# Kernel tuning notes

Hardware: AMD Instinct MI355X
Metric: run time of the kernel (lower is better)

## Reference

```python
import jax, jax.numpy as jnp
import numpy as np

N_NODES = 50000
N_EDGES = 800000
D_IN, D_HID, D_OUT = 64, 128, 64


def _glorot(key, fan_in, fan_out):
    lim = (6.0 / (fan_in + fan_out)) ** 0.5
    return jax.random.uniform(key, (fan_in, fan_out), jnp.float32, -lim, lim)


def setup_inputs() -> dict:
    key = jax.random.key(0)
    ks = jax.random.split(key, 10)
    x = jax.random.normal(ks[0], (N_NODES, D_IN), jnp.float32)
    edge_index = jax.random.randint(ks[1], (2, N_EDGES), 0, N_NODES, jnp.int64)
    # GINConv1 MLP: Linear(D_IN->D_HID), ReLU, Linear(D_HID->D_HID)
    W1a = _glorot(ks[2], D_IN, D_HID); b1a = jnp.zeros((D_HID,), jnp.float32)
    W1b = _glorot(ks[3], D_HID, D_HID); b1b = jnp.zeros((D_HID,), jnp.float32)
    # GINConv2 MLP: Linear(D_HID->D_HID), ReLU, Linear(D_HID->D_OUT)
    W2a = _glorot(ks[4], D_HID, D_HID); b2a = jnp.zeros((D_HID,), jnp.float32)
    W2b = _glorot(ks[5], D_HID, D_OUT); b2b = jnp.zeros((D_OUT,), jnp.float32)
    return {"x": x, "edge_index": edge_index,
            "W1a": W1a, "b1a": b1a, "W1b": W1b, "b1b": b1b,
            "W2a": W2a, "b2a": b2a, "W2b": W2b, "b2b": b2b}


def _gin_conv(x, src, dst, Wa, ba, Wb, bb):
    # GIN aggregation (eps = 0): h_i = x_i + sum_{j in N(i)} x_j
    msgs = x[src]                                   # [E, d] gather
    agg = jax.ops.segment_sum(msgs, dst, num_segments=x.shape[0])  # [N, d]
    h = x + agg
    # 2-layer MLP
    h = jax.nn.relu(h @ Wa + ba)
    return h @ Wb + bb


def reference(x, edge_index, W1a, b1a, W1b, b1b, W2a, b2a, W2b, b2b):
    src, dst = edge_index[0], edge_index[1]
    h = jax.nn.relu(_gin_conv(x, src, dst, W1a, b1a, W1b, b1b))
    h = jax.nn.relu(_gin_conv(h, src, dst, W2a, b2a, W2b, b2b))
    return h
```

## Files before the change

kernel.cpp:

```cpp
#include <hip/hip_runtime.h>

#define N_NODES 50000
#define N_EDGES 800000

typedef __attribute__((ext_vector_type(8))) short short8;
typedef __attribute__((ext_vector_type(4))) float floatx4;

static __device__ __forceinline__ unsigned short f2b(float f) {
    unsigned int u = __float_as_uint(f);
    unsigned int r = u + 0x7fffu + ((u >> 16) & 1u);
    return (unsigned short)(r >> 16);
}
static __device__ __forceinline__ unsigned int pk(float a, float b) {
    return (unsigned)f2b(a) | ((unsigned)f2b(b) << 16);
}
static __device__ __forceinline__ float blo(unsigned int u) {
    return __uint_as_float(u << 16);
}
static __device__ __forceinline__ float bhi(unsigned int u) {
    return __uint_as_float(u & 0xffff0000u);
}

__global__ void hist_kernel(const int* __restrict__ dst, int* __restrict__ deg,
                            int n) {
    int i = blockIdx.x * blockDim.x + threadIdx.x;
    if (i < n) atomicAdd(&deg[dst[i]], 1);
}

__global__ __launch_bounds__(1024) void scanA_kernel(
    const int* __restrict__ deg, int* __restrict__ bsum, int n) {
    __shared__ int s[1024];
    const int tid = threadIdx.x;
    int i = blockIdx.x * 1024 + tid;
    s[tid] = (i < n) ? deg[i] : 0;
    __syncthreads();
    for (int d = 512; d > 0; d >>= 1) {
        if (tid < d) s[tid] += s[tid + d];
        __syncthreads();
    }
    if (tid == 0) bsum[blockIdx.x] = s[0];
}

__global__ __launch_bounds__(64) void scanB_kernel(int* __restrict__ bsum,
                                                   int nb) {
    const int tid = threadIdx.x;
    int v = (tid < nb) ? bsum[tid] : 0;
    for (int d = 1; d < 64; d <<= 1) {
        int t = __shfl_up(v, d, 64);
        if (tid >= d) v += t;
    }
    int excl = __shfl_up(v, 1, 64);
    if (tid == 0) excl = 0;
    if (tid < nb) bsum[tid] = excl;
}

__global__ __launch_bounds__(1024) void scanC_kernel(
    const int* __restrict__ deg, const int* __restrict__ bpref,
    int* __restrict__ off, int* __restrict__ cursor, int n) {
    __shared__ int s[1024];
    const int tid = threadIdx.x;
    const int i = blockIdx.x * 1024 + tid;
    const int v = (i < n) ? deg[i] : 0;
    s[tid] = v;
    __syncthreads();
    for (int d = 1; d < 1024; d <<= 1) {
        int t = (tid >= d) ? s[tid - d] : 0;
        __syncthreads();
        s[tid] += t;
        __syncthreads();
    }
    const int excl = s[tid] - v + bpref[blockIdx.x];
    if (i < n) {
        off[i] = excl;
        cursor[i] = excl;
        if (i == n - 1) off[n] = excl + v;
    }
}

__global__ void fill_kernel(const int* __restrict__ src,
                            const int* __restrict__ dst,
                            int* __restrict__ cursor,
                            unsigned short* __restrict__ nbr, int n) {
    int i = blockIdx.x * blockDim.x + threadIdx.x;
    if (i < n) {
        int pos = atomicAdd(&cursor[dst[i]], 1);
        nbr[pos] = (unsigned short)src[i];
    }
}

__global__ __launch_bounds__(256) void prep_weights_kernel(
    const float* __restrict__ W1a, const float* __restrict__ W1b,
    const float* __restrict__ W2a, const float* __restrict__ W2b,
    unsigned short* __restrict__ W1aT, unsigned short* __restrict__ W1bT,
    unsigned short* __restrict__ W2aT, unsigned short* __restrict__ W2bT) {
    int i = blockIdx.x * 256 + threadIdx.x;
    if (i < 8192) {
        int n = i >> 6, k = i & 63;
        W1aT[i] = f2b(W1a[k * 128 + n]);
    } else if (i < 24576) {
        int j = i - 8192, n = j >> 7, k = j & 127;
        W1bT[j] = f2b(W1b[k * 128 + n]);
    } else if (i < 40960) {
        int j = i - 24576, n = j >> 7, k = j & 127;
        W2aT[j] = f2b(W2a[k * 128 + n]);
    } else if (i < 49152) {
        int j = i - 40960, n = j >> 7, k = j & 127;
        W2bT[j] = f2b(W2b[k * 64 + n]);
    }
}

__global__ __launch_bounds__(256) void convert_x_kernel(
    const float* __restrict__ x, unsigned short* __restrict__ xb, int n4) {
    int i = blockIdx.x * 256 + threadIdx.x;
    if (i < n4) {
        float4 v = ((const float4*)x)[i];
        uint2 o;
        o.x = pk(v.x, v.y);
        o.y = pk(v.z, v.w);
        ((uint2*)xb)[i] = o;
    }
}

__global__ __launch_bounds__(256) void gather1_kernel(
    const unsigned short* __restrict__ xb, const int* __restrict__ off,
    const unsigned short* __restrict__ nbr, unsigned short* __restrict__ t1,
    int n_nodes) {
    const int tid = threadIdx.x;
    const int node = blockIdx.x * 16 + (tid >> 4);
    const int c = tid & 15;
    if (node >= n_nodes) return;
    const uint2* xr = (const uint2*)xb;
    const uint2 a = xr[(size_t)node * 16 + c];
    float f0 = blo(a.x), f1 = bhi(a.x), f2 = blo(a.y), f3 = bhi(a.y);
    const int lo = off[node], hi = off[node + 1];
    int j = lo;
    for (; j + 4 <= hi; j += 4) {
        const int s0 = nbr[j], s1 = nbr[j + 1], s2 = nbr[j + 2],
                  s3 = nbr[j + 3];
        const uint2 v0 = xr[(size_t)s0 * 16 + c];
        const uint2 v1 = xr[(size_t)s1 * 16 + c];
        const uint2 v2 = xr[(size_t)s2 * 16 + c];
        const uint2 v3 = xr[(size_t)s3 * 16 + c];
        f0 += (blo(v0.x) + blo(v1.x)) + (blo(v2.x) + blo(v3.x));
        f1 += (bhi(v0.x) + bhi(v1.x)) + (bhi(v2.x) + bhi(v3.x));
        f2 += (blo(v0.y) + blo(v1.y)) + (blo(v2.y) + blo(v3.y));
        f3 += (bhi(v0.y) + bhi(v1.y)) + (bhi(v2.y) + bhi(v3.y));
    }
    for (; j < hi; ++j) {
        const uint2 v = xr[(size_t)nbr[j] * 16 + c];
        f0 += blo(v.x); f1 += bhi(v.x);
        f2 += blo(v.y); f3 += bhi(v.y);
    }
    uint2 o;
    o.x = pk(f0, f1);
    o.y = pk(f2, f3);
    ((uint2*)t1)[(size_t)node * 16 + c] = o;
}

__global__ __launch_bounds__(256) void gather2_kernel(
    const unsigned short* __restrict__ h, const int* __restrict__ off,
    const unsigned short* __restrict__ nbr, unsigned short* __restrict__ t2,
    int n_nodes) {
    const int tid = threadIdx.x;
    const int node = blockIdx.x * 16 + (tid >> 4);
    const int c = tid & 15;
    if (node >= n_nodes) return;
    const uint4* hr = (const uint4*)h;
    const uint4 a = hr[(size_t)node * 16 + c];
    float f0 = blo(a.x), f1 = bhi(a.x), f2 = blo(a.y), f3 = bhi(a.y);
    float f4 = blo(a.z), f5 = bhi(a.z), f6 = blo(a.w), f7 = bhi(a.w);
    const int lo = off[node], hi = off[node + 1];
    int j = lo;
    for (; j + 4 <= hi; j += 4) {
        const int s0 = nbr[j], s1 = nbr[j + 1], s2 = nbr[j + 2],
                  s3 = nbr[j + 3];
        const uint4 v0 = hr[(size_t)s0 * 16 + c];
        const uint4 v1 = hr[(size_t)s1 * 16 + c];
        const uint4 v2 = hr[(size_t)s2 * 16 + c];
        const uint4 v3 = hr[(size_t)s3 * 16 + c];
        f0 += (blo(v0.x) + blo(v1.x)) + (blo(v2.x) + blo(v3.x));
        f1 += (bhi(v0.x) + bhi(v1.x)) + (bhi(v2.x) + bhi(v3.x));
        f2 += (blo(v0.y) + blo(v1.y)) + (blo(v2.y) + blo(v3.y));
        f3 += (bhi(v0.y) + bhi(v1.y)) + (bhi(v2.y) + bhi(v3.y));
        f4 += (blo(v0.z) + blo(v1.z)) + (blo(v2.z) + blo(v3.z));
        f5 += (bhi(v0.z) + bhi(v1.z)) + (bhi(v2.z) + bhi(v3.z));
        f6 += (blo(v0.w) + blo(v1.w)) + (blo(v2.w) + blo(v3.w));
        f7 += (bhi(v0.w) + bhi(v1.w)) + (bhi(v2.w) + bhi(v3.w));
    }
    for (; j < hi; ++j) {
        const uint4 v = hr[(size_t)nbr[j] * 16 + c];
        f0 += blo(v.x); f1 += bhi(v.x); f2 += blo(v.y); f3 += bhi(v.y);
        f4 += blo(v.z); f5 += bhi(v.z); f6 += blo(v.w); f7 += bhi(v.w);
    }
    uint4 o;
    o.x = pk(f0, f1); o.y = pk(f2, f3);
    o.z = pk(f4, f5); o.w = pk(f6, f7);
    ((uint4*)t2)[(size_t)node * 16 + c] = o;
}

template <int DIN, int DH, int DOUT, bool OUT_BF16>
__global__ __launch_bounds__(256) void mlp_mfma_kernel(
    const unsigned short* __restrict__ t, const unsigned short* __restrict__ WaT,
    const float* __restrict__ ba, const unsigned short* __restrict__ WbT,
    const float* __restrict__ bb, void* __restrict__ outp, int n_rows) {
    constexpr int SA = DIN + 16;
    constexpr int SH = DH + 16;
    __shared__ unsigned short tA[64 * SA];
    __shared__ unsigned short hidA[64 * SH];

    const int tid = threadIdx.x;
    const int row0 = blockIdx.x * 64;

    constexpr int CHUNKS = 64 * DIN / 8;
    const uint4* tg = (const uint4*)t;
    for (int i = tid; i < CHUNKS; i += 256) {
        const int row = i / (DIN / 8);
        const int cb = i % (DIN / 8);
        uint4 v = {0u, 0u, 0u, 0u};
        const int gr = row0 + row;
        if (gr < n_rows) v = tg[(size_t)gr * (DIN / 8) + cb];
        *(uint4*)&tA[row * SA + cb * 8] = v;
    }
    __syncthreads();

    const int lane = tid & 63;
    const int wv = tid >> 6;
    const int quad = lane >> 4;
    const int l16 = lane & 15;
    const int m0 = wv * 16;

    short8 a1[DIN / 32];
#pragma unroll
    for (int kk = 0; kk < DIN / 32; ++kk)
        a1[kk] = *(const short8*)&tA[(m0 + l16) * SA + kk * 32 + quad * 8];
#pragma unroll
    for (int nt = 0; nt < DH / 16; ++nt) {
        floatx4 acc = {0.f, 0.f, 0.f, 0.f};
#pragma unroll
        for (int kk = 0; kk < DIN / 32; ++kk) {
            short8 b =
                *(const short8*)&WaT[(nt * 16 + l16) * DIN + kk * 32 + quad * 8];
            acc = __builtin_amdgcn_mfma_f32_16x16x32_bf16(a1[kk], b, acc, 0, 0, 0);
        }
        const float bias = ba[nt * 16 + l16];
#pragma unroll
        for (int r = 0; r < 4; ++r) {
            const float v = fmaxf(acc[r] + bias, 0.f);
            hidA[(m0 + quad * 4 + r) * SH + nt * 16 + l16] = f2b(v);
        }
    }

    short8 a2[DH / 32];
#pragma unroll
    for (int kk = 0; kk < DH / 32; ++kk)
        a2[kk] = *(const short8*)&hidA[(m0 + l16) * SH + kk * 32 + quad * 8];
#pragma unroll
    for (int nt = 0; nt < DOUT / 16; ++nt) {
        floatx4 acc = {0.f, 0.f, 0.f, 0.f};
#pragma unroll
        for (int kk = 0; kk < DH / 32; ++kk) {
            short8 b =
                *(const short8*)&WbT[(nt * 16 + l16) * DH + kk * 32 + quad * 8];
            acc = __builtin_amdgcn_mfma_f32_16x16x32_bf16(a2[kk], b, acc, 0, 0, 0);
        }
        const float bias = bb[nt * 16 + l16];
#pragma unroll
        for (int r = 0; r < 4; ++r) {
            const float v = fmaxf(acc[r] + bias, 0.f);
            const int grow = row0 + m0 + quad * 4 + r;
            if (grow < n_rows) {
                if (OUT_BF16)
                    ((unsigned short*)outp)[(size_t)grow * DOUT + nt * 16 + l16] =
                        f2b(v);
                else
                    ((float*)outp)[(size_t)grow * DOUT + nt * 16 + l16] = v;
            }
        }
    }
}

extern "C" void kernel_launch(void* const* d_in, const int* in_sizes, int n_in,
                              void* d_out, int out_size, void* d_ws,
                              size_t ws_size, hipStream_t stream) {
    const float* x   = (const float*)d_in[0];
    const int*   ei  = (const int*)d_in[1];
    const float* W1a = (const float*)d_in[2];
    const float* b1a = (const float*)d_in[3];
    const float* W1b = (const float*)d_in[4];
    const float* b1b = (const float*)d_in[5];
    const float* W2a = (const float*)d_in[6];
    const float* b2a = (const float*)d_in[7];
    const float* W2b = (const float*)d_in[8];
    const float* b2b = (const float*)d_in[9];
    float* out = (float*)d_out;

    const int* src = ei;
    const int* dst = ei + N_EDGES;

    unsigned short* xb = (unsigned short*)d_ws;
    unsigned short* t1 = xb + (size_t)N_NODES * 64;
    unsigned short* h  = t1 + (size_t)N_NODES * 64;
    unsigned short* t2 = h + (size_t)N_NODES * 128;
    unsigned short* W1aT = t2 + (size_t)N_NODES * 128;
    unsigned short* W1bT = W1aT + 8192;
    unsigned short* W2aT = W1bT + 16384;
    unsigned short* W2bT = W2aT + 16384;
    int* deg    = (int*)(W2bT + 8192);
    int* off    = deg + N_NODES;
    int* cursor = off + N_NODES + 1;
    int* bsum   = cursor + N_NODES;
    unsigned short* nbr = (unsigned short*)(bsum + 64);

    constexpr int NB = (N_NODES + 1023) / 1024;

    hipMemsetAsync(deg, 0, N_NODES * sizeof(int), stream);
    hist_kernel<<<(N_EDGES + 255) / 256, 256, 0, stream>>>(dst, deg, N_EDGES);
    scanA_kernel<<<NB, 1024, 0, stream>>>(deg, bsum, N_NODES);
    scanB_kernel<<<1, 64, 0, stream>>>(bsum, NB);
    scanC_kernel<<<NB, 1024, 0, stream>>>(deg, bsum, off, cursor, N_NODES);
    fill_kernel<<<(N_EDGES + 255) / 256, 256, 0, stream>>>(src, dst, cursor,
                                                           nbr, N_EDGES);
    prep_weights_kernel<<<192, 256, 0, stream>>>(W1a, W1b, W2a, W2b, W1aT,
                                                 W1bT, W2aT, W2bT);
    convert_x_kernel<<<(N_NODES * 16 + 255) / 256, 256, 0, stream>>>(
        x, xb, N_NODES * 16);

    gather1_kernel<<<(N_NODES + 15) / 16, 256, 0, stream>>>(xb, off, nbr, t1,
                                                            N_NODES);
    mlp_mfma_kernel<64, 128, 128, true>
        <<<(N_NODES + 63) / 64, 256, 0, stream>>>(t1, W1aT, b1a, W1bT, b1b, h,
                                                  N_NODES);

    gather2_kernel<<<(N_NODES + 15) / 16, 256, 0, stream>>>(h, off, nbr, t2,
                                                            N_NODES);
    mlp_mfma_kernel<128, 128, 64, false>
        <<<(N_NODES + 63) / 64, 256, 0, stream>>>(t2, W2aT, b2a, W2bT, b2b, out,
                                                  N_NODES);
}
```

Measured before the change: 271.2 us.

## Partition CSR histogram/fill atomics by destination range and fuse small prep kernels

The histogram and fill kernels now split the destination-node space into 8 ranges. Each block scans a chunk of edges but only issues atomics for destinations in its range, so concurrent atomics and scattered writes land in a narrower region (intended for better L2 locality). The single-block scan kernel is removed: each scanC block sums the earlier block totals serially. Weight transposition and x conversion are merged into one launch. The cost is reading dst (and src for fill) eight times, plus a serial prefix loop in each scan block.

```diff
diff --git a/kernel.cpp b/kernel.cpp
--- a/kernel.cpp
+++ b/kernel.cpp
@@ -2,6 +2,8 @@
 
 #define N_NODES 50000
 #define N_EDGES 800000
+#define N_SG 8
+#define DST_PER_SG (N_NODES / N_SG)
 
 typedef __attribute__((ext_vector_type(8))) short short8;
 typedef __attribute__((ext_vector_type(4))) float floatx4;
@@ -21,10 +23,19 @@
     return __uint_as_float(u & 0xffff0000u);
 }
 
-__global__ void hist_kernel(const int* __restrict__ dst, int* __restrict__ deg,
-                            int n) {
-    int i = blockIdx.x * blockDim.x + threadIdx.x;
-    if (i < n) atomicAdd(&deg[dst[i]], 1);
+__global__ __launch_bounds__(256) void hist_part_kernel(
+    const int* __restrict__ dst, int* __restrict__ deg, int n) {
+    const int sg = blockIdx.x & (N_SG - 1);
+    const int cb = blockIdx.x >> 3;
+    const int nchunks = gridDim.x >> 3;
+    const int chunk = (n + nchunks - 1) / nchunks;
+    const int lo = cb * chunk;
+    const int hi = min(lo + chunk, n);
+    const int dlo = sg * DST_PER_SG, dhi = dlo + DST_PER_SG;
+    for (int e = lo + threadIdx.x; e < hi; e += 256) {
+        const int d = dst[e];
+        if (d >= dlo && d < dhi) atomicAdd(&deg[d], 1);
+    }
 }
 
 __global__ __launch_bounds__(1024) void scanA_kernel(
@@ -41,24 +52,17 @@
     if (tid == 0) bsum[blockIdx.x] = s[0];
 }
 
-__global__ __launch_bounds__(64) void scanB_kernel(int* __restrict__ bsum,
-                                                   int nb) {
-    const int tid = threadIdx.x;
-    int v = (tid < nb) ? bsum[tid] : 0;
-    for (int d = 1; d < 64; d <<= 1) {
-        int t = __shfl_up(v, d, 64);
-        if (tid >= d) v += t;
-    }
-    int excl = __shfl_up(v, 1, 64);
-    if (tid == 0) excl = 0;
-    if (tid < nb) bsum[tid] = excl;
-}
-
 __global__ __launch_bounds__(1024) void scanC_kernel(
-    const int* __restrict__ deg, const int* __restrict__ bpref,
+    const int* __restrict__ deg, const int* __restrict__ bsum,
     int* __restrict__ off, int* __restrict__ cursor, int n) {
     __shared__ int s[1024];
-    const int tid = threadIdx.x;
+    __shared__ int bpref;
+    const int tid = threadIdx.x;
+    if (tid == 0) {
+        int p = 0;
+        for (int j = 0; j < blockIdx.x; ++j) p += bsum[j];
+        bpref = p;
+    }
     const int i = blockIdx.x * 1024 + tid;
     const int v = (i < n) ? deg[i] : 0;
     s[tid] = v;
@@ -69,7 +73,7 @@
         s[tid] += t;
         __syncthreads();
     }
-    const int excl = s[tid] - v + bpref[blockIdx.x];
+    const int excl = s[tid] - v + bpref;
     if (i < n) {
         off[i] = excl;
         cursor[i] = excl;
@@ -77,22 +81,31 @@
     }
 }
 
-__global__ void fill_kernel(const int* __restrict__ src,
-                            const int* __restrict__ dst,
-                            int* __restrict__ cursor,
-                            unsigned short* __restrict__ nbr, int n) {
-    int i = blockIdx.x * blockDim.x + threadIdx.x;
-    if (i < n) {
-        int pos = atomicAdd(&cursor[dst[i]], 1);
-        nbr[pos] = (unsigned short)src[i];
-    }
-}
-
-__global__ __launch_bounds__(256) void prep_weights_kernel(
+__global__ __launch_bounds__(256) void fill_part_kernel(
+    const int* __restrict__ src, const int* __restrict__ dst,
+    int* __restrict__ cursor, unsigned short* __restrict__ nbr, int n) {
+    const int sg = blockIdx.x & (N_SG - 1);
+    const int cb = blockIdx.x >> 3;
+    const int nchunks = gridDim.x >> 3;
+    const int chunk = (n + nchunks - 1) / nchunks;
+    const int lo = cb * chunk;
+    const int hi = min(lo + chunk, n);
+    const int dlo = sg * DST_PER_SG, dhi = dlo + DST_PER_SG;
+    for (int e = lo + threadIdx.x; e < hi; e += 256) {
+        const int d = dst[e];
+        if (d >= dlo && d < dhi) {
+            int pos = atomicAdd(&cursor[d], 1);
+            nbr[pos] = (unsigned short)src[e];
+        }
+    }
+}
+
+__global__ __launch_bounds__(256) void prep_kernel(
     const float* __restrict__ W1a, const float* __restrict__ W1b,
     const float* __restrict__ W2a, const float* __restrict__ W2b,
-    unsigned short* __restrict__ W1aT, unsigned short* __restrict__ W1bT,
-    unsigned short* __restrict__ W2aT, unsigned short* __restrict__ W2bT) {
+    const float* __restrict__ x, unsigned short* __restrict__ W1aT,
+    unsigned short* __restrict__ W1bT, unsigned short* __restrict__ W2aT,
+    unsigned short* __restrict__ W2bT, unsigned short* __restrict__ xb) {
     int i = blockIdx.x * 256 + threadIdx.x;
     if (i < 8192) {
         int n = i >> 6, k = i & 63;
@@ -106,18 +119,15 @@
     } else if (i < 49152) {
         int j = i - 40960, n = j >> 7, k = j & 127;
         W2bT[j] = f2b(W2b[k * 64 + n]);
-    }
-}
-
-__global__ __launch_bounds__(256) void convert_x_kernel(
-    const float* __restrict__ x, unsigned short* __restrict__ xb, int n4) {
-    int i = blockIdx.x * 256 + threadIdx.x;
-    if (i < n4) {
-        float4 v = ((const float4*)x)[i];
-        uint2 o;
-        o.x = pk(v.x, v.y);
-        o.y = pk(v.z, v.w);
-        ((uint2*)xb)[i] = o;
+    } else {
+        int j = i - 49152;
+        if (j < N_NODES * 16) {
+            float4 v = ((const float4*)x)[j];
+            uint2 o;
+            o.x = pk(v.x, v.y);
+            o.y = pk(v.z, v.w);
+            ((uint2*)xb)[j] = o;
+        }
     }
 }
 
@@ -314,16 +324,12 @@
     constexpr int NB = (N_NODES + 1023) / 1024;
 
     hipMemsetAsync(deg, 0, N_NODES * sizeof(int), stream);
-    hist_kernel<<<(N_EDGES + 255) / 256, 256, 0, stream>>>(dst, deg, N_EDGES);
+    hist_part_kernel<<<1024, 256, 0, stream>>>(dst, deg, N_EDGES);
     scanA_kernel<<<NB, 1024, 0, stream>>>(deg, bsum, N_NODES);
-    scanB_kernel<<<1, 64, 0, stream>>>(bsum, NB);
     scanC_kernel<<<NB, 1024, 0, stream>>>(deg, bsum, off, cursor, N_NODES);
-    fill_kernel<<<(N_EDGES + 255) / 256, 256, 0, stream>>>(src, dst, cursor,
-                                                           nbr, N_EDGES);
-    prep_weights_kernel<<<192, 256, 0, stream>>>(W1a, W1b, W2a, W2b, W1aT,
-                                                 W1bT, W2aT, W2bT);
-    convert_x_kernel<<<(N_NODES * 16 + 255) / 256, 256, 0, stream>>>(
-        x, xb, N_NODES * 16);
+    fill_part_kernel<<<1024, 256, 0, stream>>>(src, dst, cursor, nbr, N_EDGES);
+    prep_kernel<<<(49152 + N_NODES * 16 + 255) / 256, 256, 0, stream>>>(
+        W1a, W1b, W2a, W2b, x, W1aT, W1bT, W2aT, W2bT, xb);
 
     gather1_kernel<<<(N_NODES + 15) / 16, 256, 0, stream>>>(xb, off, nbr, t1,
                                                             N_NODES);
```

Measured after the change: 267.1 us. Within noise of the previous version (-1.5%).
